# Optimization experiments

Measured on AMD Instinct MI355X. Metric: run time of the kernel, lower is better.

The kernel has to match this reference:

```python
import jax, jax.numpy as jnp
import numpy as np

B, DV, W, H = 128, 2048, 14, 14
S = W * H            # 196 spatial positions
DQ = 2048            # question vector dim
DA = 1200            # attention dim_v == dim_q == dim_mm (MLB elementwise fusion)
G = 4                # nb_glimpses
DH = 2048            # fusion dim_h (total); per-glimpse = DH // G
NANS = 3000


def setup_inputs() -> dict:
    key = jax.random.key(0)
    ks = jax.random.split(key, 16)
    s = 0.02
    return {
        "input_v": jax.random.normal(ks[0], (B, DV, W, H), jnp.float32),
        "x_q_vec": jax.random.normal(ks[1], (B, DQ), jnp.float32),
        # conv_v_att: 1x1 conv DV->DA  (expressed as channel matmul)
        "Wv_att": jax.random.normal(ks[2], (DV, DA), jnp.float32) * s,
        "bv_att": jnp.zeros((DA,), jnp.float32),
        # linear_q_att: DQ->DA
        "Wq_att": jax.random.normal(ks[3], (DQ, DA), jnp.float32) * s,
        "bq_att": jnp.zeros((DA,), jnp.float32),
        # conv_att: 1x1 conv DA->G
        "Wa": jax.random.normal(ks[4], (DA, G), jnp.float32) * s,
        "ba": jnp.zeros((G,), jnp.float32),
        # per-glimpse fusion linears DV -> DH//G, stacked over glimpses
        "Wf": jax.random.normal(ks[5], (G, DV, DH // G), jnp.float32) * s,
        "bf": jnp.zeros((G, DH // G), jnp.float32),
        # linear_q_fusion: DQ -> DH
        "Wqf": jax.random.normal(ks[6], (DQ, DH), jnp.float32) * s,
        "bqf": jnp.zeros((DH,), jnp.float32),
        # linear_classif: DH -> NANS
        "Wc": jax.random.normal(ks[7], (DH, NANS), jnp.float32) * s,
        "bc": jnp.zeros((NANS,), jnp.float32),
    }


def reference(input_v, x_q_vec, Wv_att, bv_att, Wq_att, bq_att, Wa, ba,
              Wf, bf, Wqf, bqf, Wc, bc):
    b = input_v.shape[0]
    v_flat = input_v.reshape(b, DV, S)                      # [B, DV, S]

    # --- attention scores ---
    # conv_v_att (1x1) + tanh -> [B, S, DA]
    x_v = jnp.tanh(jnp.einsum('bcs,cd->bsd', v_flat, Wv_att) + bv_att)
    # linear_q_att + tanh -> [B, DA], broadcast over spatial
    x_q = jnp.tanh(x_q_vec @ Wq_att + bq_att)
    # MLB fusion_att: elementwise multiply, then tanh (activation_mm)
    x_att = jnp.tanh(x_v * x_q[:, None, :])                 # [B, S, DA]
    scores = jnp.einsum('bsd,dg->bsg', x_att, Wa) + ba      # [B, S, G]
    att = jax.nn.softmax(scores, axis=1)                    # softmax over spatial

    # --- weighted pooling per glimpse ---
    v_att = jnp.einsum('bsg,bcs->bgc', att, v_flat)         # [B, G, DV]

    # --- fusion of glimpses ---
    xv = jnp.tanh(jnp.einsum('bgc,gch->bgh', v_att, Wf) + bf)  # [B, G, DH/G]
    xv = xv.reshape(b, DH)                                   # concat glimpses
    xq = jnp.tanh(x_q_vec @ Wqf + bqf)                       # [B, DH]
    x = xv * xq                                              # MLB fusion_classif

    # --- classifier ---
    x = jnp.tanh(x)
    return x @ Wc + bc                                       # [B, NANS]
```

## Files before the change

### kernel.cpp

```cpp
#include <hip/hip_runtime.h>
#include <hip/hip_bf16.h>

#define BB   128
#define DV   2048
#define SS   196
#define DQ   2048
#define DA   1200
#define DAP  1280
#define GG   4
#define DH   2048
#define NANS 3000
#define NANSP 3008
#define MROWS (BB*SS)
#define NT   5
#define KSPLIT 8
#define KCHUNK (DV/KSPLIT)
#define NQ   (DAP + DH)

typedef __attribute__((ext_vector_type(8))) short bf16x8;
typedef __attribute__((ext_vector_type(4))) float f32x4;

__device__ __forceinline__ float fast_tanh(float x) {
    float e = __expf(2.0f * x);
    return 1.0f - 2.0f * __builtin_amdgcn_rcpf(e + 1.0f);
}

__device__ __forceinline__ void async_copy16(const void* gsrc, void* ldst) {
    __builtin_amdgcn_global_load_lds(
        (const __attribute__((address_space(1))) void*)gsrc,
        (__attribute__((address_space(3))) void*)ldst, 16, 0, 0);
}

__global__ __launch_bounds__(256) void transpose_v(const float* __restrict__ v,
                                                   __hip_bfloat16* __restrict__ vt) {
    const int b    = blockIdx.z;
    const int t    = threadIdx.x;
    const int lane = t & 63;
    const int w    = t >> 6;
    const int sl   = lane >> 2;
    const int cq   = lane & 3;
    const int s    = blockIdx.y * 16 + sl;
    const int c0   = blockIdx.x * 128 + w * 32 + cq * 8;
    if (s >= SS) return;
    const float* src = v + (size_t)b * DV * SS + (size_t)c0 * SS + s;
    float f[8];
#pragma unroll
    for (int i = 0; i < 8; ++i) f[i] = src[(size_t)i * SS];
    union { bf16x8 v8; __hip_bfloat16 h[8]; } u;
#pragma unroll
    for (int i = 0; i < 8; ++i) u.h[i] = __float2bfloat16(f[i]);
    *(bf16x8*)(vt + ((size_t)b * SS + s) * DV + c0) = u.v8;
}

template <int SEL>
__device__ __forceinline__ void gemm_body(
    int bx, int by, int t,
    const float* __restrict__ A, int lda,
    const float* __restrict__ Bm, const float* __restrict__ B2,
    float* __restrict__ Cp, int Npad,
    float* As, float* Bs) {
    const int n0    = bx * 64;
    const int kbase = by * KCHUNK;

    const float* Aeff = A;
    const float* Beff;
    int ldb, ncol0, nlim;
    if (SEL == 0) {
        Beff = Bm; ldb = NANS; ncol0 = n0; nlim = NANS;
    } else if (SEL == 1) {
        int gg = n0 >> 9;
        Aeff = A + gg * 2048;
        Beff = Bm + (size_t)gg * 2048 * 512;
        ldb = 512; ncol0 = n0 & 511; nlim = 1 << 30;
    } else {
        if (n0 < DAP) { Beff = Bm; ldb = DA; ncol0 = n0;      nlim = DA; }
        else          { Beff = B2; ldb = DH; ncol0 = n0 - DAP; nlim = 1 << 30; }
    }

    const int tm = (t & 31) * 4;
    const int tn = (t >> 5) * 8;
    const int sm = t >> 1, kq = t & 1;
    const int bk = t >> 4, bn4 = (t & 15) * 4;
    const bool bok = (ncol0 + bn4 + 3) < nlim;
    float acc[4][8] = {};

    for (int k0 = kbase; k0 < kbase + KCHUNK; k0 += 64) {
        {
            const float* Ap = Aeff + (size_t)sm * lda + k0 + kq * 32;
#pragma unroll
            for (int i = 0; i < 8; ++i) {
                float4 a4 = *(const float4*)(Ap + i * 4);
                int kk = kq * 32 + i * 4;
                As[(kk + 0) * 132 + sm] = a4.x;
                As[(kk + 1) * 132 + sm] = a4.y;
                As[(kk + 2) * 132 + sm] = a4.z;
                As[(kk + 3) * 132 + sm] = a4.w;
            }
        }
        {
#pragma unroll
            for (int i = 0; i < 4; ++i) {
                int k = bk + i * 16;
                float4 b4 = bok
                    ? *(const float4*)(Beff + (size_t)(k0 + k) * ldb + ncol0 + bn4)
                    : (float4){0.f, 0.f, 0.f, 0.f};
                *(float4*)(Bs + k * 68 + bn4) = b4;
            }
        }
        __syncthreads();
#pragma unroll
        for (int kk = 0; kk < 64; ++kk) {
            const float4 av = *(const float4*)(As + kk * 132 + tm);
            const float4 b0 = *(const float4*)(Bs + kk * 68 + tn);
            const float4 b1 = *(const float4*)(Bs + kk * 68 + tn + 4);
            const float am[4] = {av.x, av.y, av.z, av.w};
#pragma unroll
            for (int i = 0; i < 4; ++i) {
                acc[i][0] += am[i] * b0.x; acc[i][1] += am[i] * b0.y;
                acc[i][2] += am[i] * b0.z; acc[i][3] += am[i] * b0.w;
                acc[i][4] += am[i] * b1.x; acc[i][5] += am[i] * b1.y;
                acc[i][6] += am[i] * b1.z; acc[i][7] += am[i] * b1.w;
            }
        }
        __syncthreads();
    }
#pragma unroll
    for (int i = 0; i < 4; ++i) {
        size_t base = ((size_t)by * 128 + tm + i) * Npad + n0 + tn;
        float4 v0 = {acc[i][0], acc[i][1], acc[i][2], acc[i][3]};
        float4 v1 = {acc[i][4], acc[i][5], acc[i][6], acc[i][7]};
        *(float4*)(Cp + base) = v0;
        *(float4*)(Cp + base + 4) = v1;
    }
}

template <int SEL>
__global__ __launch_bounds__(256) void gemm_partial(
    const float* __restrict__ A, int lda,
    const float* __restrict__ Bm, const float* __restrict__ B2,
    float* __restrict__ Cp, int Npad) {
    __shared__ __align__(16) float As[64 * 132];
    __shared__ __align__(16) float Bs[64 * 68];
    gemm_body<SEL>(blockIdx.x, blockIdx.y, threadIdx.x, A, lda, Bm, B2, Cp,
                   Npad, As, Bs);
}

__global__ __launch_bounds__(256) void front_pack(
    const float* __restrict__ bv, const float* __restrict__ Wa,
    float* __restrict__ bvp, float* __restrict__ wap,
    const float* __restrict__ Wv, __hip_bfloat16* __restrict__ wvt,
    const float* __restrict__ x_q, const float* __restrict__ Wq_att,
    const float* __restrict__ Wqf, float* __restrict__ Cp) {
    __shared__ __align__(16) float shmem[64 * 132 + 64 * 68];
    const int t = threadIdx.x;
    int bid = blockIdx.x;
    if (bid < 20) {
        int i = bid * 256 + t;
        if (i < DAP) bvp[i] = (i < DA) ? bv[i] : 0.f;
        if (i < DAP * GG) {
            int d = i >> 2;
            wap[i] = (d < DA) ? Wa[i] : 0.f;
        }
        return;
    }
    bid -= 20;
    if (bid < 640) {
        float (*tile)[65] = (float(*)[65])shmem;
        const int d0 = (bid % 20) * 64;
        const int c0 = (bid / 20) * 64;
        const int col  = t & 63;
        const int rowb = t >> 6;
#pragma unroll
        for (int i = 0; i < 16; ++i) {
            int c = rowb + i * 4;
            int d = d0 + col;
            tile[c][col] = (d < DA) ? Wv[(size_t)(c0 + c) * DA + d] : 0.f;
        }
        __syncthreads();
#pragma unroll
        for (int i = 0; i < 16; ++i) {
            int dl = rowb + i * 4;
            wvt[(size_t)(d0 + dl) * DV + c0 + col] = __float2bfloat16(tile[col][dl]);
        }
        return;
    }
    bid -= 640;
    gemm_body<2>(bid % 52, bid / 52, t, x_q, DQ, Wq_att, Wqf, Cp, NQ,
                 shmem, shmem + 64 * 132);
}

template <int MODE>
__global__ __launch_bounds__(256) void gemm_epilogue(
    const float* __restrict__ Cp, int Npad, int Nreal,
    const float* __restrict__ bias, const float* __restrict__ aux,
    float* __restrict__ out, int ldo) {
    int n = blockIdx.x * 256 + threadIdx.x;
    int m = blockIdx.y;
    if (n >= Npad) return;
    float s = 0.f;
#pragma unroll
    for (int ks = 0; ks < KSPLIT; ++ks)
        s += Cp[((size_t)ks * 128 + m) * Npad + n];
    if (MODE == 0) {
        if (n >= Nreal) return;
        out[(size_t)m * ldo + n] = s + bias[n];
    } else {
        float xv = fast_tanh(s + bias[n]);
        out[(size_t)m * ldo + n] = fast_tanh(xv * aux[(size_t)m * 2048 + n]);
    }
}

__global__ __launch_bounds__(256) void epilogue_q(
    const float* __restrict__ Cp,
    const float* __restrict__ bqa, const float* __restrict__ bqf,
    float* __restrict__ qatt, float* __restrict__ qfus) {
    int n = blockIdx.x * 256 + threadIdx.x;
    int m = blockIdx.y;
    if (n >= NQ) return;
    float s = 0.f;
#pragma unroll
    for (int ks = 0; ks < KSPLIT; ++ks)
        s += Cp[((size_t)ks * 128 + m) * NQ + n];
    if (n < DAP) {
        qatt[(size_t)m * DAP + n] = (n < DA) ? fast_tanh(s + bqa[n]) : 0.f;
    } else {
        int j = n - DAP;
        qfus[(size_t)m * DH + j] = fast_tanh(s + bqf[j]);
    }
}

__global__ __launch_bounds__(512, 2) void big_gemm(
    const __hip_bfloat16* __restrict__ vt,
    const __hip_bfloat16* __restrict__ wt,
    const float* __restrict__ bvp,
    const float* __restrict__ qatt,
    const float* __restrict__ wap,
    float* __restrict__ scores_p) {
    __shared__ __align__(16) char lds[131072];
    __shared__ __align__(16) float wa_s[256 * 4];
    __shared__ float qs[3 * 256];

    const int t    = threadIdx.x;
    const int lane = t & 63;
    const int w    = t >> 6;
    const int wr   = w >> 2;
    const int wc   = w & 3;

    int bid = blockIdx.x;
    int grp = bid / 40, r = bid % 40;
    int mt, nt;
    if (grp < 12) { mt = grp * 8 + (r & 7); nt = r >> 3; }
    else          { mt = 96 + (r & 1);      nt = r >> 1; }
    const int m0 = mt * 256, n0 = nt * 256;
    const int b_lo = m0 / SS;
    const int bs1  = (b_lo + 1) * SS;
    const int bs2  = (b_lo + 2) * SS;

    if (t < 256) *(float4*)(wa_s + t * 4) = *(const float4*)(wap + (n0 + t) * 4);
    {
        int j = t >> 8, c = t & 255;
        int b = b_lo + j;
        qs[t] = (b < BB) ? qatt[(size_t)b * DAP + n0 + c] : 0.f;
        if (t < 256) {
            int b2 = b_lo + 2;
            qs[512 + t] = (b2 < BB) ? qatt[(size_t)b2 * DAP + n0 + t] : 0.f;
        }
    }
    __syncthreads();

    const int srow   = t >> 2;
    const int schunk = (t & 3) ^ ((t >> 3) & 3);
    const __hip_bfloat16* aG = vt + (size_t)(m0 + srow) * DV + schunk * 8;
    const __hip_bfloat16* bG = wt + (size_t)(n0 + srow) * DV + schunk * 8;

    auto STAGE_ITEM = [&](int k, int p) {
        const int ks = p >> 1, mat = p & 1;
        const __hip_bfloat16* g = (mat ? bG : aG) + (size_t)k * 64 + ks * 32;
        char* dst = lds + (k & 1) * 65536 + ks * 32768 + mat * 16384 + t * 16;
        async_copy16(g, dst);
        async_copy16(g + (size_t)128 * DV, dst + 8192);
    };

    const int rchk = ((lane >> 4) ^ (((lane & 15) >> 1) & 3)) * 16;
    const int aRow = (wr * 128 + (lane & 15)) * 64;
    const int bRow = (wc * 64 + (lane & 15)) * 64;

    f32x4 acc[8][4];
#pragma unroll
    for (int i = 0; i < 8; ++i)
#pragma unroll
        for (int j = 0; j < 4; ++j) acc[i][j] = (f32x4){0.f, 0.f, 0.f, 0.f};

    STAGE_ITEM(0, 0); STAGE_ITEM(0, 1);
    STAGE_ITEM(0, 2); STAGE_ITEM(0, 3);
    STAGE_ITEM(1, 0);
    asm volatile("s_waitcnt vmcnt(6)" ::: "memory");
    __builtin_amdgcn_s_barrier();

    for (int kt = 0; kt < 32; ++kt) {
        const int cur = kt & 1;
        const char* Xb = lds + cur * 65536;
        bf16x8 bfr[4];
#pragma unroll
        for (int p = 0; p < 4; ++p) {
            const int ks = p >> 1, mh = p & 1;
            const char* Ar = Xb + ks * 32768;
            bf16x8 afr[4];
#pragma unroll
            for (int q = 0; q < 4; ++q)
                afr[q] = *(const bf16x8*)(Ar + aRow + (mh * 64 + q * 16) * 64 + rchk);
            if (mh == 0) {
#pragma unroll
                for (int ni = 0; ni < 4; ++ni)
                    bfr[ni] = *(const bf16x8*)(Ar + 16384 + bRow + (ni * 16) * 64 + rchk);
            }
            if (p < 3) {
                if (kt < 31) STAGE_ITEM(kt + 1, p + 1);
            } else {
                if (kt < 30) STAGE_ITEM(kt + 2, 0);
            }
            if (p == 1) {
                if (kt < 31) asm volatile("s_waitcnt vmcnt(6)" ::: "memory");
                else         asm volatile("s_waitcnt vmcnt(0)" ::: "memory");
                __builtin_amdgcn_s_barrier();
            } else if (p == 3) {
                if (kt < 30)       asm volatile("s_waitcnt vmcnt(6)" ::: "memory");
                else if (kt == 30) asm volatile("s_waitcnt vmcnt(4)" ::: "memory");
                else               asm volatile("s_waitcnt vmcnt(0)" ::: "memory");
                __builtin_amdgcn_s_barrier();
            }
            __builtin_amdgcn_s_setprio(1);
#pragma unroll
            for (int q = 0; q < 4; ++q)
#pragma unroll
                for (int ni = 0; ni < 4; ++ni)
                    acc[mh * 4 + q][ni] = __builtin_amdgcn_mfma_f32_16x16x32_bf16(
                        afr[q], bfr[ni], acc[mh * 4 + q][ni], 0, 0, 0);
            __builtin_amdgcn_s_setprio(0);
        }
    }

    __syncthreads();
    float* sc = (float*)lds;

    const int colb_l = wc * 64 + (lane & 15);
    const int colb_g = n0 + colb_l;
    float bvv[4];
    float4 wv[4];
#pragma unroll
    for (int ni = 0; ni < 4; ++ni) {
        bvv[ni] = bvp[colb_g + ni * 16];
        wv[ni]  = *(const float4*)(wa_s + (colb_l + ni * 16) * 4);
    }
#pragma unroll
    for (int mi = 0; mi < 8; ++mi) {
#pragma unroll
        for (int rr = 0; rr < 4; ++rr) {
            int lrow = wr * 128 + mi * 16 + ((lane >> 4) << 2) + rr;
            int row  = m0 + lrow;
            int qoff = (row >= bs1 ? 256 : 0) + (row >= bs2 ? 256 : 0);
            float p0 = 0.f, p1 = 0.f, p2 = 0.f, p3 = 0.f;
#pragma unroll
            for (int ni = 0; ni < 4; ++ni) {
                float xv = fast_tanh(acc[mi][ni][rr] + bvv[ni]);
                float xa = fast_tanh(xv * qs[qoff + colb_l + ni * 16]);
                p0 += xa * wv[ni].x; p1 += xa * wv[ni].y;
                p2 += xa * wv[ni].z; p3 += xa * wv[ni].w;
            }
#pragma unroll
            for (int mk = 1; mk < 16; mk <<= 1) {
                p0 += __shfl_xor(p0, mk); p1 += __shfl_xor(p1, mk);
                p2 += __shfl_xor(p2, mk); p3 += __shfl_xor(p3, mk);
            }
            if ((lane & 15) == 0)
                *(float4*)(sc + ((size_t)wc * 256 + lrow) * 4) =
                    (float4){p0, p1, p2, p3};
        }
    }
    __syncthreads();
    if (t < 256) {
        float4 s0 = *(float4*)(sc + (0 * 256 + t) * 4);
        float4 s1 = *(float4*)(sc + (1 * 256 + t) * 4);
        float4 s2 = *(float4*)(sc + (2 * 256 + t) * 4);
        float4 s3 = *(float4*)(sc + (3 * 256 + t) * 4);
        float4 s = {s0.x + s1.x + s2.x + s3.x, s0.y + s1.y + s2.y + s3.y,
                    s0.z + s1.z + s2.z + s3.z, s0.w + s1.w + s2.w + s3.w};
        *(float4*)(scores_p + ((size_t)nt * MROWS + m0 + t) * 4) = s;
    }
}

__global__ __launch_bounds__(256) void softmax_pool(
    const float* __restrict__ scores_p,
    const __hip_bfloat16* __restrict__ vt,
    float* __restrict__ vatt) {
    __shared__ __align__(16) float att[SS * GG];
    const int b = blockIdx.y;
    const int t = threadIdx.x;
    if (t < SS) {
        float4 s = {0.f, 0.f, 0.f, 0.f};
#pragma unroll
        for (int ntile = 0; ntile < NT; ++ntile) {
            float4 p = *(const float4*)(scores_p + ((size_t)ntile * MROWS + b * SS + t) * 4);
            s.x += p.x; s.y += p.y; s.z += p.z; s.w += p.w;
        }
        *(float4*)(att + t * 4) = s;
    }
    __syncthreads();
    {
        const int g = t >> 6;
        const int lane = t & 63;
        float mx = -3.0e38f;
        for (int s = lane; s < SS; s += 64) mx = fmaxf(mx, att[s * 4 + g]);
#pragma unroll
        for (int m = 32; m > 0; m >>= 1) mx = fmaxf(mx, __shfl_xor(mx, m));
        float sum = 0.f;
        for (int s = lane; s < SS; s += 64) sum += __expf(att[s * 4 + g] - mx);
#pragma unroll
        for (int m = 32; m > 0; m >>= 1) sum += __shfl_xor(sum, m);
        float inv = __builtin_amdgcn_rcpf(sum);
        for (int s = lane; s < SS; s += 64) att[s * 4 + g] = __expf(att[s * 4 + g] - mx) * inv;
    }
    __syncthreads();
    const int c = blockIdx.x * 1024 + t * 4;
    const __hip_bfloat16* vp = vt + (size_t)b * SS * DV + c;
    float a0[4] = {}, a1[4] = {}, a2[4] = {}, a3[4] = {};
#pragma unroll 4
    for (int s = 0; s < SS; ++s) {
        uint2 u = *(const uint2*)(vp + (size_t)s * DV);
        float v0 = __uint_as_float(u.x << 16);
        float v1 = __uint_as_float(u.x & 0xffff0000u);
        float v2 = __uint_as_float(u.y << 16);
        float v3 = __uint_as_float(u.y & 0xffff0000u);
        float4 aw = *(const float4*)(att + s * 4);
        a0[0] += v0 * aw.x; a0[1] += v0 * aw.y; a0[2] += v0 * aw.z; a0[3] += v0 * aw.w;
        a1[0] += v1 * aw.x; a1[1] += v1 * aw.y; a1[2] += v1 * aw.z; a1[3] += v1 * aw.w;
        a2[0] += v2 * aw.x; a2[1] += v2 * aw.y; a2[2] += v2 * aw.z; a2[3] += v2 * aw.w;
        a3[0] += v3 * aw.x; a3[1] += v3 * aw.y; a3[2] += v3 * aw.z; a3[3] += v3 * aw.w;
    }
    float* vb = vatt + (size_t)b * GG * DV;
#pragma unroll
    for (int g = 0; g < GG; ++g) {
        float4 o = {a0[g], a1[g], a2[g], a3[g]};
        *(float4*)(vb + (size_t)g * DV + c) = o;
    }
}

extern "C" void kernel_launch(void* const* d_in, const int* in_sizes, int n_in,
                              void* d_out, int out_size, void* d_ws, size_t ws_size,
                              hipStream_t stream) {
    const float* input_v = (const float*)d_in[0];
    const float* x_q     = (const float*)d_in[1];
    const float* Wv      = (const float*)d_in[2];
    const float* bv      = (const float*)d_in[3];
    const float* Wq_att  = (const float*)d_in[4];
    const float* bq_att  = (const float*)d_in[5];
    const float* Wa      = (const float*)d_in[6];
    const float* Wf      = (const float*)d_in[8];
    const float* bf_     = (const float*)d_in[9];
    const float* Wqf     = (const float*)d_in[10];
    const float* bqf     = (const float*)d_in[11];
    const float* Wc      = (const float*)d_in[12];
    const float* bc      = (const float*)d_in[13];
    float* out = (float*)d_out;

    char* wsb = (char*)d_ws;
    size_t off = 0;
    auto carve = [&](size_t bytes) -> void* {
        void* p = wsb + off;
        off += (bytes + 255) & ~(size_t)255;
        return p;
    };
    __hip_bfloat16* vt  = (__hip_bfloat16*)carve((size_t)MROWS * DV * 2);
    __hip_bfloat16* wvt = (__hip_bfloat16*)carve((size_t)DAP * DV * 2);
    float* Cp       = (float*)carve((size_t)KSPLIT * 128 * NQ * 4);
    float* scores_p = (float*)carve((size_t)NT * MROWS * GG * 4);
    float* qatt = (float*)carve((size_t)BB * DAP * 4);
    float* qfus = (float*)carve((size_t)BB * DH * 4);
    float* bvp  = (float*)carve((size_t)DAP * 4);
    float* wap  = (float*)carve((size_t)DAP * GG * 4);
    float* vatt = (float*)carve((size_t)BB * GG * DV * 4);
    float* xbuf = (float*)carve((size_t)BB * DH * 4);
    (void)ws_size; (void)n_in; (void)in_sizes; (void)out_size;

    transpose_v<<<dim3(DV / 128, 13, BB), 256, 0, stream>>>(input_v, vt);

    front_pack<<<dim3(1076), 256, 0, stream>>>(
        bv, Wa, bvp, wap, Wv, wvt, x_q, Wq_att, Wqf, Cp);
    epilogue_q<<<dim3(NQ / 256, BB), 256, 0, stream>>>(Cp, bq_att, bqf, qatt, qfus);

    big_gemm<<<dim3(490), 512, 0, stream>>>(vt, wvt, bvp, qatt, wap, scores_p);

    softmax_pool<<<dim3(2, BB), 256, 0, stream>>>(scores_p, vt, vatt);

    gemm_partial<1><<<dim3(DH / 64, KSPLIT), 256, 0, stream>>>(
        vatt, GG * DV, Wf, nullptr, Cp, DH);
    gemm_epilogue<2><<<dim3(DH / 256, BB), 256, 0, stream>>>(
        Cp, DH, DH, bf_, qfus, xbuf, DH);

    gemm_partial<0><<<dim3(NANSP / 64, KSPLIT), 256, 0, stream>>>(
        xbuf, DH, Wc, nullptr, Cp, NANSP);
    gemm_epilogue<0><<<dim3(NANSP / 256 + 1, BB), 256, 0, stream>>>(
        Cp, NANSP, NANS, bc, nullptr, out, NANS);
}
```

Measured before the change: 625.4 us.

## Merge input transpose into front kernel and hand-unroll big GEMM pipeline

```diff
diff --git a/kernel.cpp b/kernel.cpp
--- a/kernel.cpp
+++ b/kernel.cpp
@@ -31,26 +31,10 @@
         (__attribute__((address_space(3))) void*)ldst, 16, 0, 0);
 }
 
-__global__ __launch_bounds__(256) void transpose_v(const float* __restrict__ v,
-                                                   __hip_bfloat16* __restrict__ vt) {
-    const int b    = blockIdx.z;
-    const int t    = threadIdx.x;
-    const int lane = t & 63;
-    const int w    = t >> 6;
-    const int sl   = lane >> 2;
-    const int cq   = lane & 3;
-    const int s    = blockIdx.y * 16 + sl;
-    const int c0   = blockIdx.x * 128 + w * 32 + cq * 8;
-    if (s >= SS) return;
-    const float* src = v + (size_t)b * DV * SS + (size_t)c0 * SS + s;
-    float f[8];
-#pragma unroll
-    for (int i = 0; i < 8; ++i) f[i] = src[(size_t)i * SS];
-    union { bf16x8 v8; __hip_bfloat16 h[8]; } u;
-#pragma unroll
-    for (int i = 0; i < 8; ++i) u.h[i] = __float2bfloat16(f[i]);
-    *(bf16x8*)(vt + ((size_t)b * SS + s) * DV + c0) = u.v8;
-}
+#define VM6 asm volatile("s_waitcnt vmcnt(6)" ::: "memory")
+#define VM4 asm volatile("s_waitcnt vmcnt(4)" ::: "memory")
+#define VM0 asm volatile("s_waitcnt vmcnt(0)" ::: "memory")
+#define BAR __builtin_amdgcn_s_barrier()
 
 template <int SEL>
 __device__ __forceinline__ void gemm_body(
@@ -145,15 +129,43 @@
                    Npad, As, Bs);
 }
 
-__global__ __launch_bounds__(256) void front_pack(
+__global__ __launch_bounds__(256) void front(
     const float* __restrict__ bv, const float* __restrict__ Wa,
     float* __restrict__ bvp, float* __restrict__ wap,
     const float* __restrict__ Wv, __hip_bfloat16* __restrict__ wvt,
     const float* __restrict__ x_q, const float* __restrict__ Wq_att,
-    const float* __restrict__ Wqf, float* __restrict__ Cp) {
+    const float* __restrict__ Wqf, float* __restrict__ Cp,
+    const float* __restrict__ v, __hip_bfloat16* __restrict__ vt) {
     __shared__ __align__(16) float shmem[64 * 132 + 64 * 68];
     const int t = threadIdx.x;
     int bid = blockIdx.x;
+    if (bid < 416) {
+        gemm_body<2>(bid % 52, bid / 52, t, x_q, DQ, Wq_att, Wqf, Cp, NQ,
+                     shmem, shmem + 64 * 132);
+        return;
+    }
+    bid -= 416;
+    if (bid < 640) {
+        float (*tile)[65] = (float(*)[65])shmem;
+        const int d0 = (bid % 20) * 64;
+        const int c0 = (bid / 20) * 64;
+        const int col  = t & 63;
+        const int rowb = t >> 6;
+#pragma unroll
+        for (int i = 0; i < 16; ++i) {
+            int c = rowb + i * 4;
+            int d = d0 + col;
+            tile[c][col] = (d < DA) ? Wv[(size_t)(c0 + c) * DA + d] : 0.f;
+        }
+        __syncthreads();
+#pragma unroll
+        for (int i = 0; i < 16; ++i) {
+            int dl = rowb + i * 4;
+            wvt[(size_t)(d0 + dl) * DV + c0 + col] = __float2bfloat16(tile[col][dl]);
+        }
+        return;
+    }
+    bid -= 640;
     if (bid < 20) {
         int i = bid * 256 + t;
         if (i < DAP) bvp[i] = (i < DA) ? bv[i] : 0.f;
@@ -164,29 +176,26 @@
         return;
     }
     bid -= 20;
-    if (bid < 640) {
-        float (*tile)[65] = (float(*)[65])shmem;
-        const int d0 = (bid % 20) * 64;
-        const int c0 = (bid / 20) * 64;
-        const int col  = t & 63;
-        const int rowb = t >> 6;
-#pragma unroll
-        for (int i = 0; i < 16; ++i) {
-            int c = rowb + i * 4;
-            int d = d0 + col;
-            tile[c][col] = (d < DA) ? Wv[(size_t)(c0 + c) * DA + d] : 0.f;
-        }
-        __syncthreads();
-#pragma unroll
-        for (int i = 0; i < 16; ++i) {
-            int dl = rowb + i * 4;
-            wvt[(size_t)(d0 + dl) * DV + c0 + col] = __float2bfloat16(tile[col][dl]);
-        }
-        return;
-    }
-    bid -= 640;
-    gemm_body<2>(bid % 52, bid / 52, t, x_q, DQ, Wq_att, Wqf, Cp, NQ,
-                 shmem, shmem + 64 * 132);
+    {
+        const int cx = bid & 15;
+        const int sy = (bid >> 4) % 13;
+        const int b  = bid / 208;
+        const int lane = t & 63;
+        const int w    = t >> 6;
+        const int sl   = lane >> 2;
+        const int cq   = lane & 3;
+        const int s    = sy * 16 + sl;
+        const int c0   = cx * 128 + w * 32 + cq * 8;
+        if (s >= SS) return;
+        const float* src = v + (size_t)b * DV * SS + (size_t)c0 * SS + s;
+        float f[8];
+#pragma unroll
+        for (int i = 0; i < 8; ++i) f[i] = src[(size_t)i * SS];
+        union { bf16x8 v8; __hip_bfloat16 h[8]; } u;
+#pragma unroll
+        for (int i = 0; i < 8; ++i) u.h[i] = __float2bfloat16(f[i]);
+        *(bf16x8*)(vt + ((size_t)b * SS + s) * DV + c0) = u.v8;
+    }
 }
 
 template <int MODE>
@@ -270,20 +279,21 @@
 
     const int srow   = t >> 2;
     const int schunk = (t & 3) ^ ((t >> 3) & 3);
-    const __hip_bfloat16* aG = vt + (size_t)(m0 + srow) * DV + schunk * 8;
-    const __hip_bfloat16* bG = wt + (size_t)(n0 + srow) * DV + schunk * 8;
-
-    auto STAGE_ITEM = [&](int k, int p) {
-        const int ks = p >> 1, mat = p & 1;
-        const __hip_bfloat16* g = (mat ? bG : aG) + (size_t)k * 64 + ks * 32;
-        char* dst = lds + (k & 1) * 65536 + ks * 32768 + mat * 16384 + t * 16;
+    const __hip_bfloat16* aS = vt + (size_t)(m0 + srow) * DV + schunk * 8;
+    const __hip_bfloat16* bS = wt + (size_t)(n0 + srow) * DV + schunk * 8;
+    char* dst0 = lds + t * 16;
+
+    auto ST = [&](const __hip_bfloat16* gbase, int goff, char* dst) {
+        const char* g = (const char*)gbase + goff;
         async_copy16(g, dst);
-        async_copy16(g + (size_t)128 * DV, dst + 8192);
+        async_copy16(g + (size_t)128 * DV * 2, dst + 8192);
     };
 
     const int rchk = ((lane >> 4) ^ (((lane & 15) >> 1) & 3)) * 16;
     const int aRow = (wr * 128 + (lane & 15)) * 64;
     const int bRow = (wc * 64 + (lane & 15)) * 64;
+    const char* A0 = lds;
+    const char* A1 = lds + 65536;
 
     f32x4 acc[8][4];
 #pragma unroll
@@ -291,54 +301,89 @@
 #pragma unroll
         for (int j = 0; j < 4; ++j) acc[i][j] = (f32x4){0.f, 0.f, 0.f, 0.f};
 
-    STAGE_ITEM(0, 0); STAGE_ITEM(0, 1);
-    STAGE_ITEM(0, 2); STAGE_ITEM(0, 3);
-    STAGE_ITEM(1, 0);
-    asm volatile("s_waitcnt vmcnt(6)" ::: "memory");
-    __builtin_amdgcn_s_barrier();
-
-    for (int kt = 0; kt < 32; ++kt) {
-        const int cur = kt & 1;
-        const char* Xb = lds + cur * 65536;
-        bf16x8 bfr[4];
-#pragma unroll
-        for (int p = 0; p < 4; ++p) {
-            const int ks = p >> 1, mh = p & 1;
-            const char* Ar = Xb + ks * 32768;
-            bf16x8 afr[4];
-#pragma unroll
-            for (int q = 0; q < 4; ++q)
-                afr[q] = *(const bf16x8*)(Ar + aRow + (mh * 64 + q * 16) * 64 + rchk);
-            if (mh == 0) {
-#pragma unroll
-                for (int ni = 0; ni < 4; ++ni)
-                    bfr[ni] = *(const bf16x8*)(Ar + 16384 + bRow + (ni * 16) * 64 + rchk);
-            }
-            if (p < 3) {
-                if (kt < 31) STAGE_ITEM(kt + 1, p + 1);
-            } else {
-                if (kt < 30) STAGE_ITEM(kt + 2, 0);
-            }
-            if (p == 1) {
-                if (kt < 31) asm volatile("s_waitcnt vmcnt(6)" ::: "memory");
-                else         asm volatile("s_waitcnt vmcnt(0)" ::: "memory");
-                __builtin_amdgcn_s_barrier();
-            } else if (p == 3) {
-                if (kt < 30)       asm volatile("s_waitcnt vmcnt(6)" ::: "memory");
-                else if (kt == 30) asm volatile("s_waitcnt vmcnt(4)" ::: "memory");
-                else               asm volatile("s_waitcnt vmcnt(0)" ::: "memory");
-                __builtin_amdgcn_s_barrier();
-            }
-            __builtin_amdgcn_s_setprio(1);
-#pragma unroll
-            for (int q = 0; q < 4; ++q)
-#pragma unroll
-                for (int ni = 0; ni < 4; ++ni)
-                    acc[mh * 4 + q][ni] = __builtin_amdgcn_mfma_f32_16x16x32_bf16(
-                        afr[q], bfr[ni], acc[mh * 4 + q][ni], 0, 0, 0);
-            __builtin_amdgcn_s_setprio(0);
-        }
-    }
+    auto HALF_A = [&](const char* Ar, int mh, bf16x8* afr) {
+#pragma unroll
+        for (int q = 0; q < 4; ++q)
+            afr[q] = *(const bf16x8*)(Ar + aRow + (mh * 64 + q * 16) * 64 + rchk);
+    };
+    auto HALF_B = [&](const char* Ar, bf16x8* bfr) {
+#pragma unroll
+        for (int ni = 0; ni < 4; ++ni)
+            bfr[ni] = *(const bf16x8*)(Ar + 16384 + bRow + (ni * 16) * 64 + rchk);
+    };
+    auto MF = [&](int mh, bf16x8* afr, bf16x8* bfr) {
+        __builtin_amdgcn_s_setprio(1);
+#pragma unroll
+        for (int q = 0; q < 4; ++q)
+#pragma unroll
+            for (int ni = 0; ni < 4; ++ni)
+                acc[mh * 4 + q][ni] = __builtin_amdgcn_mfma_f32_16x16x32_bf16(
+                    afr[q], bfr[ni], acc[mh * 4 + q][ni], 0, 0, 0);
+        __builtin_amdgcn_s_setprio(0);
+    };
+
+#define TILE8(XB, NXT, SAME, G1, G2, WA, WB)                                   \
+    {                                                                          \
+        bf16x8 afr[4], bfr[4];                                                 \
+        HALF_A((XB), 0, afr); HALF_B((XB), bfr);                               \
+        ST(bS, (G1), dst0 + (NXT) + 16384);                                    \
+        MF(0, afr, bfr);                                                       \
+        HALF_A((XB), 1, afr);                                                  \
+        ST(aS, (G1) + 64, dst0 + (NXT) + 32768);                               \
+        WA; BAR;                                                               \
+        MF(1, afr, bfr);                                                       \
+        HALF_A((XB) + 32768, 0, afr); HALF_B((XB) + 32768, bfr);               \
+        ST(bS, (G1) + 64, dst0 + (NXT) + 49152);                               \
+        MF(0, afr, bfr);                                                       \
+        HALF_A((XB) + 32768, 1, afr);                                          \
+        ST(aS, (G2), dst0 + (SAME));                                           \
+        WB; BAR;                                                               \
+        MF(1, afr, bfr);                                                       \
+    }
+
+    ST(aS, 0,   dst0 + 0);
+    ST(bS, 0,   dst0 + 16384);
+    ST(aS, 64,  dst0 + 32768);
+    ST(bS, 64,  dst0 + 49152);
+    ST(aS, 128, dst0 + 65536);
+    VM6;
+    BAR;
+
+    for (int it = 0; it < 15; ++it) {
+        TILE8(A0, 65536, 0, 128, 256, VM6, VM6);
+        TILE8(A1, 0, 65536, 256, 384, VM6, VM6);
+        aS += 128; bS += 128;
+    }
+    {
+        bf16x8 afr[4], bfr[4];
+        HALF_A(A0, 0, afr); HALF_B(A0, bfr);
+        ST(bS, 128, dst0 + 65536 + 16384);
+        MF(0, afr, bfr);
+        HALF_A(A0, 1, afr);
+        ST(aS, 192, dst0 + 65536 + 32768);
+        VM6; BAR;
+        MF(1, afr, bfr);
+        HALF_A(A0 + 32768, 0, afr); HALF_B(A0 + 32768, bfr);
+        ST(bS, 192, dst0 + 65536 + 49152);
+        MF(0, afr, bfr);
+        HALF_A(A0 + 32768, 1, afr);
+        VM4; BAR;
+        MF(1, afr, bfr);
+    }
+    {
+        bf16x8 afr[4], bfr[4];
+        HALF_A(A1, 0, afr); HALF_B(A1, bfr);
+        MF(0, afr, bfr);
+        HALF_A(A1, 1, afr);
+        VM0; BAR;
+        MF(1, afr, bfr);
+        HALF_A(A1 + 32768, 0, afr); HALF_B(A1 + 32768, bfr);
+        MF(0, afr, bfr);
+        HALF_A(A1 + 32768, 1, afr);
+        VM0; BAR;
+        MF(1, afr, bfr);
+    }
+#undef TILE8
 
     __syncthreads();
     float* sc = (float*)lds;
@@ -482,10 +527,8 @@
     float* xbuf = (float*)carve((size_t)BB * DH * 4);
     (void)ws_size; (void)n_in; (void)in_sizes; (void)out_size;
 
-    transpose_v<<<dim3(DV / 128, 13, BB), 256, 0, stream>>>(input_v, vt);
-
-    front_pack<<<dim3(1076), 256, 0, stream>>>(
-        bv, Wa, bvp, wap, Wv, wvt, x_q, Wq_att, Wqf, Cp);
+    front<<<dim3(416 + 640 + 20 + 26624), 256, 0, stream>>>(
+        bv, Wa, bvp, wap, Wv, wvt, x_q, Wq_att, Wqf, Cp, input_v, vt);
     epilogue_q<<<dim3(NQ / 256, BB), 256, 0, stream>>>(Cp, bq_att, bqf, qatt, qfus);
 
     big_gemm<<<dim3(490), 512, 0, stream>>>(vt, wvt, bvp, qatt, wap, scores_p);
```

Measured after the change: 653.6 us. 1.05x slower.
